# Kernel tuning notes

Hardware: AMD Instinct MI355X
Metric: run time of the kernel (lower is better)

The kernel has to match this reference:

```python
import jax, jax.numpy as jnp
import numpy as np

B, N, H = 2, 4096, 2048
NH, HD = 16, 128
BLK = 256
EPS = 1e-6


def setup_inputs() -> dict:
    key = jax.random.key(0)
    ks = jax.random.split(key, 5)
    scale = 0.02
    x = jax.random.normal(ks[0], (B, N, H), dtype=jnp.float32)
    # ALiBi-style per-head slopes, shape [h,1,1]
    slopes = (1.0 / (2.0 ** (8.0 * np.arange(1, NH + 1) / NH))).astype(np.float32)
    slope_rate = jnp.asarray(slopes).reshape(NH, 1, 1)
    w_qkv = jax.random.normal(ks[1], (3 * NH * HD, H), dtype=jnp.float32) * scale
    w_gate = jax.random.normal(ks[2], (NH * HD, H), dtype=jnp.float32) * scale
    w_out = jax.random.normal(ks[3], (H, NH * HD), dtype=jnp.float32) * scale
    norm_w = jnp.ones((NH * HD,), dtype=jnp.float32)
    return {"hidden_states": x, "slope_rate": slope_rate, "w_qkv": w_qkv,
            "w_gate": w_gate, "w_out": w_out, "norm_w": norm_w}


def _lightning_attn(x, slope_rate, w_qkv, w_gate, w_out, norm_w):
    b, n, _ = x.shape
    h, d = NH, HD
    nb = n // BLK
    # qkv projection + activation
    qkv = jax.nn.silu(jnp.einsum('bnf,of->bno', x, w_qkv))        # [b,n,3hd]
    qkv = qkv.reshape(b, n, h, 3 * d)
    q, k, v = jnp.split(qkv, 3, axis=-1)                          # each [b,n,h,d]
    q = q.transpose(0, 2, 1, 3)                                   # [b,h,n,d]
    k = k.transpose(0, 2, 1, 3)
    v = v.transpose(0, 2, 1, 3)

    s = slope_rate.astype(jnp.float32)                            # [h,1,1]
    arr = jnp.arange(1, BLK + 1, dtype=jnp.float32)               # 1..BLOCK
    q_decay = jnp.exp(-s * arr[:, None])                          # [h,BLK,1]
    k_decay = jnp.exp(-s * (BLK - arr)[:, None])                  # [h,BLK,1]
    idx = arr[:, None] - arr[None, :]                             # [BLK,BLK]
    diag_decay = jnp.where(idx >= 0, jnp.exp(-s * idx), 0.0)      # [h,BLK,BLK]
    block_decay = jnp.exp(-s * BLK)                               # [h,1,1]

    # split sequence into blocks; scan axis leading
    qb = q.reshape(b, h, nb, BLK, d).transpose(2, 0, 1, 3, 4)     # [nb,b,h,BLK,d]
    kb = k.reshape(b, h, nb, BLK, d).transpose(2, 0, 1, 3, 4)
    vb = v.reshape(b, h, nb, BLK, d).transpose(2, 0, 1, 3, 4)

    def step(kv, blk):
        qi, ki, vi = blk                                          # [b,h,BLK,d]
        o_inter = jnp.einsum('bhmd,bhde->bhme', qi * q_decay, kv)
        qk = jnp.einsum('bhmd,bhnd->bhmn', qi, ki) * diag_decay
        o_intra = jnp.einsum('bhmn,bhne->bhme', qk, vi)
        kv_new = block_decay * kv + jnp.einsum('bhmd,bhme->bhde', ki * k_decay, vi)
        return kv_new, o_inter + o_intra

    kv0 = jnp.zeros((b, h, d, d), dtype=jnp.float32)
    _, out = jax.lax.scan(step, kv0, (qb, kb, vb))                # [nb,b,h,BLK,d]
    out = out.transpose(1, 2, 0, 3, 4).reshape(b, h, n, d)        # [b,h,n,d]
    out = out.transpose(0, 2, 1, 3).reshape(b, n, h * d)          # [b,n,h*d]

    # RMSNorm (fp32)
    var = jnp.mean(out * out, axis=-1, keepdims=True)
    out = norm_w * (out * jax.lax.rsqrt(var + EPS))

    gate = jax.nn.sigmoid(jnp.einsum('bnf,of->bno', x, w_gate))
    return jnp.einsum('bno,fo->bnf', gate * out, w_out)


def reference(hidden_states, slope_rate, w_qkv, w_gate, w_out, norm_w):
    return _lightning_attn(hidden_states, slope_rate, w_qkv, w_gate, w_out, norm_w)
```

## Files before the change

### kernel.cpp

```cpp
#include <hip/hip_runtime.h>
#include <hip/hip_bf16.h>
#include <stdint.h>


typedef __bf16 bf16_t;
typedef __bf16 bf16x8 __attribute__((ext_vector_type(8)));
typedef __bf16 bf16x4 __attribute__((ext_vector_type(4)));
typedef float  f32x4  __attribute__((ext_vector_type(4)));

#define AS1C(p) ((const __attribute__((address_space(1))) void*)(p))
#define AS3(p)  ((__attribute__((address_space(3))) void*)(p))

__global__ __launch_bounds__(256)
void cvt4_kernel(const float* __restrict__ s0, bf16_t* __restrict__ d0, int n0,
                 const float* __restrict__ s1, bf16_t* __restrict__ d1, int n1,
                 const float* __restrict__ s2, bf16_t* __restrict__ d2, int n2,
                 const float* __restrict__ s3, bf16_t* __restrict__ d3, int n3) {
    const int total = n0 + n1 + n2 + n3;
    const int stride = gridDim.x * blockDim.x;
    for (int i = blockIdx.x * blockDim.x + threadIdx.x; i < total; i += stride) {
        const float* s; bf16_t* d; int j = i;
        if (j < n0) { s = s0; d = d0; }
        else {
            j -= n0;
            if (j < n1) { s = s1; d = d1; }
            else {
                j -= n1;
                if (j < n2) { s = s2; d = d2; }
                else { j -= n2; s = s3; d = d3; }
            }
        }
        float4 v = ((const float4*)s)[j];
        bf16x4 o;
        o[0] = (bf16_t)v.x; o[1] = (bf16_t)v.y; o[2] = (bf16_t)v.z; o[3] = (bf16_t)v.w;
        ((bf16x4*)d)[j] = o;
    }
}

template <int EPI>
__global__ __launch_bounds__(512)
void gemm6(const bf16_t* __restrict__ A, const bf16_t* __restrict__ Bm,
           int M, int N, int K,
           float* __restrict__ outf, bf16_t* __restrict__ outb,
           bf16_t* __restrict__ qb, bf16_t* __restrict__ kb,
           bf16_t* __restrict__ kT, bf16_t* __restrict__ vT,
           const float* __restrict__ slopes) {
    __shared__ char lds[2][65536];
    const int tid = threadIdx.x, w = tid >> 6, lane = tid & 63;
    const int l15 = lane & 15, lq = lane >> 4;
    const int wr = w >> 2, wc = w & 3;

    const int nwg = gridDim.x;
    const int cpx = nwg >> 3;
    const int id = blockIdx.x;
    const int sw = (id & 7) * cpx + (id >> 3);
    const int gx = N >> 8;
    const int tm = (sw / gx) << 8;
    const int tn = (sw % gx) << 8;
    const int nt = K >> 6;

    auto stageA1 = [&](char* dst, int t1, int j) {
        const bf16_t* base = A + (size_t)tm * K + t1 * 64;
        const int c = tid + j * 512;
        const int r = c >> 3, sl = c & 7;
        __builtin_amdgcn_global_load_lds(
            AS1C(base + (size_t)r * K + ((sl ^ (r & 7)) << 3)),
            AS3(dst + c * 16), 16, 0, 0);
    };
    auto stageB1 = [&](char* dst, int t1, int j) {
        const bf16_t* base = Bm + (size_t)tn * K + t1 * 64;
        const int c = tid + j * 512;
        const int r = c >> 3, sl = c & 7;
        __builtin_amdgcn_global_load_lds(
            AS1C(base + (size_t)r * K + ((sl ^ (r & 7)) << 3)),
            AS3(dst + 32768 + c * 16), 16, 0, 0);
    };

    f32x4 acc[8][4] = {};

    {
        char* d0 = &lds[0][0];
        stageA1(d0, 0, 0); stageA1(d0, 0, 1); stageA1(d0, 0, 2); stageA1(d0, 0, 3);
        stageB1(d0, 0, 0); stageB1(d0, 0, 1); stageB1(d0, 0, 2); stageB1(d0, 0, 3);
    }

    for (int t = 0; t < nt; ++t) {
        const char* cur = &lds[t & 1][0];
        char* nxt = &lds[1 - (t & 1)][0];
        const bool pre = (t + 1 < nt);

        asm volatile("s_waitcnt vmcnt(0)" ::: "memory");
        __builtin_amdgcn_s_barrier();
        __builtin_amdgcn_sched_barrier(0);

        bf16x8 bfr[4][2], af[4][2];
#pragma unroll
        for (int n = 0; n < 4; ++n)
#pragma unroll
            for (int kk = 0; kk < 2; ++kk) {
                const int row = wc * 64 + n * 16 + l15;
                bfr[n][kk] = *(const bf16x8*)(cur + 32768 + row * 128 + ((((kk << 2) | lq) ^ (row & 7)) << 4));
            }
#pragma unroll
        for (int m = 0; m < 4; ++m)
#pragma unroll
            for (int kk = 0; kk < 2; ++kk) {
                const int row = wr * 128 + m * 16 + l15;
                af[m][kk] = *(const bf16x8*)(cur + row * 128 + ((((kk << 2) | lq) ^ (row & 7)) << 4));
            }
        if (pre) {
            stageA1(nxt, t + 1, 0); stageA1(nxt, t + 1, 1);
            stageA1(nxt, t + 1, 2); stageA1(nxt, t + 1, 3);
            stageB1(nxt, t + 1, 0); stageB1(nxt, t + 1, 1);
            stageB1(nxt, t + 1, 2); stageB1(nxt, t + 1, 3);
        }
        __builtin_amdgcn_s_setprio(1);
#pragma unroll
        for (int m = 0; m < 4; ++m)
#pragma unroll
            for (int n = 0; n < 4; ++n)
#pragma unroll
                for (int kk = 0; kk < 2; ++kk)
                    acc[m][n] = __builtin_amdgcn_mfma_f32_16x16x32_bf16(af[m][kk], bfr[n][kk], acc[m][n], 0, 0, 0);
        __builtin_amdgcn_s_setprio(0);

#pragma unroll
        for (int m = 0; m < 4; ++m)
#pragma unroll
            for (int kk = 0; kk < 2; ++kk) {
                const int row = wr * 128 + 64 + m * 16 + l15;
                af[m][kk] = *(const bf16x8*)(cur + row * 128 + ((((kk << 2) | lq) ^ (row & 7)) << 4));
            }
        __builtin_amdgcn_s_setprio(1);
#pragma unroll
        for (int m = 0; m < 4; ++m)
#pragma unroll
            for (int n = 0; n < 4; ++n)
#pragma unroll
                for (int kk = 0; kk < 2; ++kk)
                    acc[4 + m][n] = __builtin_amdgcn_mfma_f32_16x16x32_bf16(af[m][kk], bfr[n][kk], acc[4 + m][n], 0, 0, 0);
        __builtin_amdgcn_s_setprio(0);
    }

#pragma unroll
    for (int m = 0; m < 8; ++m) {
#pragma unroll
        for (int n = 0; n < 4; ++n) {
            const int colb = tn + wc * 64 + n * 16;
            if (EPI == 2) {
#pragma unroll
                for (int r = 0; r < 4; ++r) {
                    const int row = tm + wr * 128 + m * 16 + lq * 4 + r;
                    outf[(size_t)row * N + colb + l15] = acc[m][n][r];
                }
            } else if (EPI == 1) {
#pragma unroll
                for (int r = 0; r < 4; ++r) {
                    const int row = tm + wr * 128 + m * 16 + lq * 4 + r;
                    const float v = acc[m][n][r];
                    outb[(size_t)row * N + colb + l15] = (bf16_t)(1.f / (1.f + __expf(-v)));
                }
            } else {
                const int head = colb / 384;
                const int jj = colb % 384;
                const int row0 = tm + wr * 128 + m * 16 + lq * 4;
                const int bidx = row0 >> 12;
                const int nn0 = row0 & 4095;
                const size_t bh = (size_t)(bidx * 16 + head);
                float sv[4];
#pragma unroll
                for (int r = 0; r < 4; ++r) {
                    const float v = acc[m][n][r];
                    sv[r] = v / (1.f + __expf(-v));
                }
                if (jj < 128) {
                    bf16_t* qp = qb + (bh * 4096 + nn0) * 128 + jj + l15;
#pragma unroll
                    for (int r = 0; r < 4; ++r) qp[(size_t)r * 128] = (bf16_t)sv[r];
                } else if (jj < 256) {
                    bf16_t* kp = kb + (bh * 4096 + nn0) * 128 + (jj - 128) + l15;
#pragma unroll
                    for (int r = 0; r < 4; ++r) kp[(size_t)r * 128] = (bf16_t)sv[r];
                    bf16x4 pk;
#pragma unroll
                    for (int r = 0; r < 4; ++r) pk[r] = (bf16_t)sv[r];
                    *(bf16x4*)(kT + bh * 524288 + (size_t)(jj - 128 + l15) * 4096 + nn0) = pk;
                } else {
                    bf16x4 pv;
#pragma unroll
                    for (int r = 0; r < 4; ++r) pv[r] = (bf16_t)sv[r];
                    *(bf16x4*)(vT + bh * 524288 + (size_t)(jj - 256 + l15) * 4096 + nn0) = pv;
                }
            }
        }
    }
}

__global__ __launch_bounds__(256)
void pass_ct(const bf16_t* __restrict__ vT, const bf16_t* __restrict__ kT,
             float* __restrict__ CT, const float* __restrict__ slopes) {
    const int idx = blockIdx.x, bh = idx >> 4, j = idx & 15;
    const float s = slopes[bh & 15];
    const int tid = threadIdx.x, w = tid >> 6, lane = tid & 63;
    const int l15 = lane & 15, lq = lane >> 4;
    const int we = (w & 1) * 64, wd = (w >> 1) * 64;
    const bf16_t* va = vT + (size_t)bh * 524288 + j * 256;
    const bf16_t* ka = kT + (size_t)bh * 524288 + j * 256;
    f32x4 acc[4][4] = {};
#pragma unroll
    for (int kk = 0; kk < 8; ++kk) {
        float fdec[8];
#pragma unroll
        for (int t = 0; t < 8; ++t)
            fdec[t] = __expf(-s * (float)(255 - (kk * 32 + lq * 8 + t)));
        bf16x8 af[4], bfv[4];
#pragma unroll
        for (int et = 0; et < 4; ++et)
            af[et] = *(const bf16x8*)(va + (size_t)(we + et * 16 + l15) * 4096 + kk * 32 + lq * 8);
#pragma unroll
        for (int dt = 0; dt < 4; ++dt) {
            bf16x8 raw = *(const bf16x8*)(ka + (size_t)(wd + dt * 16 + l15) * 4096 + kk * 32 + lq * 8);
#pragma unroll
            for (int t = 0; t < 8; ++t) bfv[dt][t] = (bf16_t)((float)raw[t] * fdec[t]);
        }
#pragma unroll
        for (int et = 0; et < 4; ++et)
#pragma unroll
            for (int dt = 0; dt < 4; ++dt)
                acc[et][dt] = __builtin_amdgcn_mfma_f32_16x16x32_bf16(af[et], bfv[dt], acc[et][dt], 0, 0, 0);
    }
    float* out = CT + (size_t)idx * 16384;
#pragma unroll
    for (int et = 0; et < 4; ++et)
#pragma unroll
        for (int dt = 0; dt < 4; ++dt)
#pragma unroll
            for (int r = 0; r < 4; ++r)
                out[(size_t)(we + et * 16 + lq * 4 + r) * 128 + wd + dt * 16 + l15] = acc[et][dt][r];
}

__global__ __launch_bounds__(256)
void scan_kv(const float* __restrict__ CT, bf16_t* __restrict__ states,
             const float* __restrict__ slopes) {
    const int gid = blockIdx.x * 256 + threadIdx.x;
    const int bh = gid >> 14, elem = gid & 16383;
    const float s = slopes[bh & 15];
    const float bd = __expf(-s * 256.f);
    const float* c = CT + (size_t)bh * 16 * 16384 + elem;
    bf16_t* st = states + (size_t)bh * 16 * 16384 + elem;
    float kv = 0.f;
#pragma unroll
    for (int j = 0; j < 16; ++j) {
        st[(size_t)j * 16384] = (bf16_t)kv;
        kv = bd * kv + c[(size_t)j * 16384];
    }
}

__global__ __launch_bounds__(512)
void pass_attn(const bf16_t* __restrict__ qb, const bf16_t* __restrict__ kb,
               const bf16_t* __restrict__ vT, const bf16_t* __restrict__ states,
               const float* __restrict__ slopes, float* __restrict__ outattn) {
    __shared__ bf16_t scratch[8][16][40];
    const int idx = blockIdx.x, bh = idx >> 4, j = idx & 15;
    const int b = bh >> 4, h = bh & 15;
    const int tid = threadIdx.x, w = tid >> 6, lane = tid & 63;
    const int l15 = lane & 15, lq = lane >> 4;
    const float s = slopes[h];
    f32x4 o[2][8] = {};
    float rowf[4];
#pragma unroll
    for (int r = 0; r < 4; ++r) rowf[r] = __expf(-s * (float)(lq * 4 + r));

    const size_t qrow = (size_t)bh * 4096 + j * 256;
    const bf16_t* qbase = qb + qrow * 128;
    const bf16_t* kbp = kb + qrow * 128;
    const bf16_t* vtp = vT + (size_t)bh * 524288 + (size_t)j * 256;

#pragma unroll
    for (int gi = 0; gi < 2; ++gi) {
        const int gg = gi ? (15 - w) : w;
        const bf16_t* qg = qbase + (size_t)(gg * 16) * 128;
        bf16x8 qf[4];
#pragma unroll
        for (int kq = 0; kq < 4; ++kq)
            qf[kq] = *(const bf16x8*)(qg + (size_t)l15 * 128 + kq * 32 + lq * 8);
        const int ncmax = gg >> 1;
        for (int nc = 0; nc <= ncmax; ++nc) {
            f32x4 sacc[2] = {};
#pragma unroll
            for (int kq = 0; kq < 4; ++kq) {
                bf16x8 b0 = *(const bf16x8*)(kbp + (size_t)(nc * 32 + l15) * 128 + kq * 32 + lq * 8);
                bf16x8 b1 = *(const bf16x8*)(kbp + (size_t)(nc * 32 + 16 + l15) * 128 + kq * 32 + lq * 8);
                sacc[0] = __builtin_amdgcn_mfma_f32_16x16x32_bf16(qf[kq], b0, sacc[0], 0, 0, 0);
                sacc[1] = __builtin_amdgcn_mfma_f32_16x16x32_bf16(qf[kq], b1, sacc[1], 0, 0, 0);
            }
#pragma unroll
            for (int nt = 0; nt < 2; ++nt) {
                const float colf = __expf(s * (float)(nc * 32 + nt * 16 + l15 - gg * 16));
#pragma unroll
                for (int r = 0; r < 4; ++r) {
                    const int mloc = lq * 4 + r;
                    const int nglob = nc * 32 + nt * 16 + l15;
                    const float f = (gg * 16 + mloc >= nglob) ? rowf[r] * colf : 0.f;
                    scratch[w][mloc][nt * 16 + l15] = (bf16_t)(sacc[nt][r] * f);
                }
            }
            bf16x8 sa = *(const bf16x8*)&scratch[w][l15][lq * 8];
            __builtin_amdgcn_s_setprio(1);
#pragma unroll
            for (int et = 0; et < 8; ++et) {
                bf16x8 bv = *(const bf16x8*)(vtp + (size_t)(et * 16 + l15) * 4096 + nc * 32 + lq * 8);
                o[gi][et] = __builtin_amdgcn_mfma_f32_16x16x32_bf16(sa, bv, o[gi][et], 0, 0, 0);
            }
            __builtin_amdgcn_s_setprio(0);
        }
    }

    float rq[2];
    rq[0] = __expf(-s * (float)(w * 16 + l15 + 1));
    rq[1] = __expf(-s * (float)((15 - w) * 16 + l15 + 1));
    const bf16_t* st = states + (size_t)idx * 16384;
#pragma unroll
    for (int kq = 0; kq < 4; ++kq) {
        bf16x8 aq[2];
#pragma unroll
        for (int gi = 0; gi < 2; ++gi) {
            const int gg = gi ? (15 - w) : w;
            bf16x8 raw = *(const bf16x8*)(qbase + (size_t)(gg * 16 + l15) * 128 + kq * 32 + lq * 8);
#pragma unroll
            for (int t = 0; t < 8; ++t) aq[gi][t] = (bf16_t)((float)raw[t] * rq[gi]);
        }
        __builtin_amdgcn_s_setprio(1);
#pragma unroll
        for (int et = 0; et < 8; ++et) {
            bf16x8 bs = *(const bf16x8*)(st + (size_t)(et * 16 + l15) * 128 + kq * 32 + lq * 8);
            o[0][et] = __builtin_amdgcn_mfma_f32_16x16x32_bf16(aq[0], bs, o[0][et], 0, 0, 0);
            o[1][et] = __builtin_amdgcn_mfma_f32_16x16x32_bf16(aq[1], bs, o[1][et], 0, 0, 0);
        }
        __builtin_amdgcn_s_setprio(0);
    }

    float* opb = outattn + ((size_t)b * 4096 + j * 256) * 2048 + h * 128;
#pragma unroll
    for (int gi = 0; gi < 2; ++gi) {
        const int gg = gi ? (15 - w) : w;
#pragma unroll
        for (int et = 0; et < 8; ++et)
#pragma unroll
            for (int r = 0; r < 4; ++r)
                opb[(size_t)(gg * 16 + lq * 4 + r) * 2048 + et * 16 + l15] = o[gi][et][r];
    }
}

__global__ __launch_bounds__(256)
void rmsnorm_gate(const float* __restrict__ attn, const bf16_t* __restrict__ gate_s,
                  const float* __restrict__ norm_w, bf16_t* __restrict__ gout) {
    const int row = blockIdx.x, tid = threadIdx.x;
    const float* ap = attn + (size_t)row * 2048 + tid * 8;
    float4 v0 = *(const float4*)(ap);
    float4 v1 = *(const float4*)(ap + 4);
    float av[8] = {v0.x, v0.y, v0.z, v0.w, v1.x, v1.y, v1.z, v1.w};
    float ss = 0.f;
#pragma unroll
    for (int i = 0; i < 8; ++i) ss += av[i] * av[i];
#pragma unroll
    for (int off = 32; off; off >>= 1) ss += __shfl_xor(ss, off);
    __shared__ float red[4];
    if ((tid & 63) == 0) red[tid >> 6] = ss;
    __syncthreads();
    const float rr = rsqrtf((red[0] + red[1] + red[2] + red[3]) * (1.0f / 2048.f) + 1e-6f);
    const bf16x8 g = *(const bf16x8*)(gate_s + (size_t)row * 2048 + tid * 8);
    const float* nw = norm_w + tid * 8;
    bf16x8 res;
#pragma unroll
    for (int i = 0; i < 8; ++i) res[i] = (bf16_t)((float)g[i] * nw[i] * av[i] * rr);
    *(bf16x8*)(gout + (size_t)row * 2048 + tid * 8) = res;
}

extern "C" void kernel_launch(void* const* d_in, const int* in_sizes, int n_in,
                              void* d_out, int out_size, void* d_ws, size_t ws_size,
                              hipStream_t stream) {
    (void)in_sizes; (void)n_in; (void)out_size;
    const float* x      = (const float*)d_in[0];
    const float* slopes = (const float*)d_in[1];
    const float* w_qkv  = (const float*)d_in[2];
    const float* w_gate = (const float*)d_in[3];
    const float* w_out  = (const float*)d_in[4];
    const float* norm_w = (const float*)d_in[5];
    float* out = (float*)d_out;
    char* ws = (char*)d_ws;

    size_t off = 0;
    auto alloc = [&](size_t bytes) { char* p = ws + off; off += (bytes + 255) & ~(size_t)255; return p; };
    bf16_t* xb     = (bf16_t*)alloc(8192ull * 2048 * 2);
    bf16_t* wqkvb  = (bf16_t*)alloc(6144ull * 2048 * 2);
    bf16_t* wgateb = (bf16_t*)alloc(2048ull * 2048 * 2);
    bf16_t* woutb  = (bf16_t*)alloc(2048ull * 2048 * 2);
    bf16_t* qb     = (bf16_t*)alloc(33554432);
    bf16_t* kb     = (bf16_t*)alloc(33554432);
    char*   ctbuf  = alloc(33554432);
    bf16_t* vT     = (bf16_t*)alloc(33554432);
    bf16_t* kT     = (bf16_t*)alloc(33554432);
    if (ws_size < off) return;
    float*  CT     = (float*)ctbuf;
    bf16_t* gate_s = kT;
    bf16_t* states = (bf16_t*)wqkvb;
    bf16_t* gout   = qb;

    cvt4_kernel<<<2048, 256, 0, stream>>>(
        x,      xb,     8192 * 2048 / 4,
        w_qkv,  wqkvb,  6144 * 2048 / 4,
        w_gate, wgateb, 2048 * 2048 / 4,
        w_out,  woutb,  2048 * 2048 / 4);
    gemm6<0><<<768, 512, 0, stream>>>(xb, wqkvb, 8192, 6144, 2048,
        nullptr, nullptr, qb, kb, kT, vT, slopes);
    pass_ct<<<512, 256, 0, stream>>>(vT, kT, CT, slopes);
    gemm6<1><<<256, 512, 0, stream>>>(xb, wgateb, 8192, 2048, 2048,
        nullptr, gate_s, nullptr, nullptr, nullptr, nullptr, nullptr);
    scan_kv<<<2048, 256, 0, stream>>>(CT, states, slopes);
    pass_attn<<<512, 512, 0, stream>>>(qb, kb, vT, states, slopes, out);
    rmsnorm_gate<<<8192, 256, 0, stream>>>(out, gate_s, norm_w, gout);
    gemm6<2><<<256, 512, 0, stream>>>(gout, woutb, 8192, 2048, 2048,
        out, nullptr, nullptr, nullptr, nullptr, nullptr, nullptr);
}
```

Baseline: 506.3 us.

## Fuse gate GEMM into QKV GEMM and store attention output as bf16

The gate projection is folded into the QKV GEMM by running one 8192-wide GEMM over the contiguous wqkv and wgate bf16 buffers. Columns at or beyond 6144 get a sigmoid epilogue written to the gate buffer; the rest keep the SiLU q/k/v scatter. The attention output is now stored as bf16 instead of fp32 and read back as bf16 by the RMSNorm kernel, halving that intermediate's traffic at some cost in precision. pass_ct replaces per-element exps with a geometric recurrence, and workspace buffers are reassigned (CT and the attention scratch now live in the output buffer).

```diff
diff --git a/kernel.cpp b/kernel.cpp
--- a/kernel.cpp
+++ b/kernel.cpp
@@ -153,43 +153,45 @@
                     const int row = tm + wr * 128 + m * 16 + lq * 4 + r;
                     outf[(size_t)row * N + colb + l15] = acc[m][n][r];
                 }
-            } else if (EPI == 1) {
-#pragma unroll
-                for (int r = 0; r < 4; ++r) {
-                    const int row = tm + wr * 128 + m * 16 + lq * 4 + r;
-                    const float v = acc[m][n][r];
-                    outb[(size_t)row * N + colb + l15] = (bf16_t)(1.f / (1.f + __expf(-v)));
-                }
             } else {
-                const int head = colb / 384;
-                const int jj = colb % 384;
-                const int row0 = tm + wr * 128 + m * 16 + lq * 4;
-                const int bidx = row0 >> 12;
-                const int nn0 = row0 & 4095;
-                const size_t bh = (size_t)(bidx * 16 + head);
-                float sv[4];
-#pragma unroll
-                for (int r = 0; r < 4; ++r) {
-                    const float v = acc[m][n][r];
-                    sv[r] = v / (1.f + __expf(-v));
-                }
-                if (jj < 128) {
-                    bf16_t* qp = qb + (bh * 4096 + nn0) * 128 + jj + l15;
-#pragma unroll
-                    for (int r = 0; r < 4; ++r) qp[(size_t)r * 128] = (bf16_t)sv[r];
-                } else if (jj < 256) {
-                    bf16_t* kp = kb + (bh * 4096 + nn0) * 128 + (jj - 128) + l15;
-#pragma unroll
-                    for (int r = 0; r < 4; ++r) kp[(size_t)r * 128] = (bf16_t)sv[r];
-                    bf16x4 pk;
-#pragma unroll
-                    for (int r = 0; r < 4; ++r) pk[r] = (bf16_t)sv[r];
-                    *(bf16x4*)(kT + bh * 524288 + (size_t)(jj - 128 + l15) * 4096 + nn0) = pk;
+                if (colb >= 6144) {
+#pragma unroll
+                    for (int r = 0; r < 4; ++r) {
+                        const int row = tm + wr * 128 + m * 16 + lq * 4 + r;
+                        const float v = acc[m][n][r];
+                        outb[(size_t)row * 2048 + (colb - 6144) + l15] = (bf16_t)(1.f / (1.f + __expf(-v)));
+                    }
                 } else {
-                    bf16x4 pv;
-#pragma unroll
-                    for (int r = 0; r < 4; ++r) pv[r] = (bf16_t)sv[r];
-                    *(bf16x4*)(vT + bh * 524288 + (size_t)(jj - 256 + l15) * 4096 + nn0) = pv;
+                    const int head = colb / 384;
+                    const int jj = colb % 384;
+                    const int row0 = tm + wr * 128 + m * 16 + lq * 4;
+                    const int bidx = row0 >> 12;
+                    const int nn0 = row0 & 4095;
+                    const size_t bh = (size_t)(bidx * 16 + head);
+                    float sv[4];
+#pragma unroll
+                    for (int r = 0; r < 4; ++r) {
+                        const float v = acc[m][n][r];
+                        sv[r] = v / (1.f + __expf(-v));
+                    }
+                    if (jj < 128) {
+                        bf16_t* qp = qb + (bh * 4096 + nn0) * 128 + jj + l15;
+#pragma unroll
+                        for (int r = 0; r < 4; ++r) qp[(size_t)r * 128] = (bf16_t)sv[r];
+                    } else if (jj < 256) {
+                        bf16_t* kp = kb + (bh * 4096 + nn0) * 128 + (jj - 128) + l15;
+#pragma unroll
+                        for (int r = 0; r < 4; ++r) kp[(size_t)r * 128] = (bf16_t)sv[r];
+                        bf16x4 pk;
+#pragma unroll
+                        for (int r = 0; r < 4; ++r) pk[r] = (bf16_t)sv[r];
+                        *(bf16x4*)(kT + bh * 524288 + (size_t)(jj - 128 + l15) * 4096 + nn0) = pk;
+                    } else {
+                        bf16x4 pv;
+#pragma unroll
+                        for (int r = 0; r < 4; ++r) pv[r] = (bf16_t)sv[r];
+                        *(bf16x4*)(vT + bh * 524288 + (size_t)(jj - 256 + l15) * 4096 + nn0) = pv;
+                    }
                 }
             }
         }
@@ -201,6 +203,7 @@
              float* __restrict__ CT, const float* __restrict__ slopes) {
     const int idx = blockIdx.x, bh = idx >> 4, j = idx & 15;
     const float s = slopes[bh & 15];
+    const float r_ = __expf(s);
     const int tid = threadIdx.x, w = tid >> 6, lane = tid & 63;
     const int l15 = lane & 15, lq = lane >> 4;
     const int we = (w & 1) * 64, wd = (w >> 1) * 64;
@@ -210,9 +213,9 @@
 #pragma unroll
     for (int kk = 0; kk < 8; ++kk) {
         float fdec[8];
-#pragma unroll
-        for (int t = 0; t < 8; ++t)
-            fdec[t] = __expf(-s * (float)(255 - (kk * 32 + lq * 8 + t)));
+        fdec[0] = __expf(-s * (float)(255 - (kk * 32 + lq * 8)));
+#pragma unroll
+        for (int t = 1; t < 8; ++t) fdec[t] = fdec[t - 1] * r_;
         bf16x8 af[4], bfv[4];
 #pragma unroll
         for (int et = 0; et < 4; ++et)
@@ -259,7 +262,7 @@
 __global__ __launch_bounds__(512)
 void pass_attn(const bf16_t* __restrict__ qb, const bf16_t* __restrict__ kb,
                const bf16_t* __restrict__ vT, const bf16_t* __restrict__ states,
-               const float* __restrict__ slopes, float* __restrict__ outattn) {
+               const float* __restrict__ slopes, bf16_t* __restrict__ outattn) {
     __shared__ bf16_t scratch[8][16][40];
     const int idx = blockIdx.x, bh = idx >> 4, j = idx & 15;
     const int b = bh >> 4, h = bh & 15;
@@ -340,7 +343,7 @@
         __builtin_amdgcn_s_setprio(0);
     }
 
-    float* opb = outattn + ((size_t)b * 4096 + j * 256) * 2048 + h * 128;
+    bf16_t* opb = outattn + ((size_t)b * 4096 + j * 256) * 2048 + h * 128;
 #pragma unroll
     for (int gi = 0; gi < 2; ++gi) {
         const int gg = gi ? (15 - w) : w;
@@ -348,18 +351,18 @@
         for (int et = 0; et < 8; ++et)
 #pragma unroll
             for (int r = 0; r < 4; ++r)
-                opb[(size_t)(gg * 16 + lq * 4 + r) * 2048 + et * 16 + l15] = o[gi][et][r];
+                opb[(size_t)(gg * 16 + lq * 4 + r) * 2048 + et * 16 + l15] = (bf16_t)o[gi][et][r];
     }
 }
 
 __global__ __launch_bounds__(256)
-void rmsnorm_gate(const float* __restrict__ attn, const bf16_t* __restrict__ gate_s,
+void rmsnorm_gate(const bf16_t* __restrict__ attn, const bf16_t* __restrict__ gate_s,
                   const float* __restrict__ norm_w, bf16_t* __restrict__ gout) {
     const int row = blockIdx.x, tid = threadIdx.x;
-    const float* ap = attn + (size_t)row * 2048 + tid * 8;
-    float4 v0 = *(const float4*)(ap);
-    float4 v1 = *(const float4*)(ap + 4);
-    float av[8] = {v0.x, v0.y, v0.z, v0.w, v1.x, v1.y, v1.z, v1.w};
+    const bf16x8 a8 = *(const bf16x8*)(attn + (size_t)row * 2048 + tid * 8);
+    float av[8];
+#pragma unroll
+    for (int i = 0; i < 8; ++i) av[i] = (float)a8[i];
     float ss = 0.f;
 #pragma unroll
     for (int i = 0; i < 8; ++i) ss += av[i] * av[i];
@@ -402,8 +405,9 @@
     bf16_t* vT     = (bf16_t*)alloc(33554432);
     bf16_t* kT     = (bf16_t*)alloc(33554432);
     if (ws_size < off) return;
-    float*  CT     = (float*)ctbuf;
-    bf16_t* gate_s = kT;
+    bf16_t* gate_s = (bf16_t*)ctbuf;
+    float*  CT     = (float*)out;
+    bf16_t* attn_s = (bf16_t*)out;
     bf16_t* states = (bf16_t*)wqkvb;
     bf16_t* gout   = qb;
 
@@ -412,14 +416,12 @@
         w_qkv,  wqkvb,  6144 * 2048 / 4,
         w_gate, wgateb, 2048 * 2048 / 4,
         w_out,  woutb,  2048 * 2048 / 4);
-    gemm6<0><<<768, 512, 0, stream>>>(xb, wqkvb, 8192, 6144, 2048,
-        nullptr, nullptr, qb, kb, kT, vT, slopes);
+    gemm6<0><<<1024, 512, 0, stream>>>(xb, wqkvb, 8192, 8192, 2048,
+        nullptr, gate_s, qb, kb, kT, vT, slopes);
     pass_ct<<<512, 256, 0, stream>>>(vT, kT, CT, slopes);
-    gemm6<1><<<256, 512, 0, stream>>>(xb, wgateb, 8192, 2048, 2048,
-        nullptr, gate_s, nullptr, nullptr, nullptr, nullptr, nullptr);
     scan_kv<<<2048, 256, 0, stream>>>(CT, states, slopes);
-    pass_attn<<<512, 512, 0, stream>>>(qb, kb, vT, states, slopes, out);
-    rmsnorm_gate<<<8192, 256, 0, stream>>>(out, gate_s, norm_w, gout);
+    pass_attn<<<512, 512, 0, stream>>>(qb, kb, vT, states, slopes, attn_s);
+    rmsnorm_gate<<<8192, 256, 0, stream>>>(attn_s, gate_s, norm_w, gout);
     gemm6<2><<<256, 512, 0, stream>>>(gout, woutb, 8192, 2048, 2048,
         out, nullptr, nullptr, nullptr, nullptr, nullptr, nullptr);
 }
```

Result: slower. 517.4 us (+2.2%).
